# Optimization experiments

Hardware: AMD Instinct MI355X
Metric: run time of the kernel (lower is better)

## Reference

```python
import jax, jax.numpy as jnp
import numpy as np

B, K, M = 16384, 256, 50
NUM_USER, NUM_ITEM, NUM_TAG = 100000, 100000, 50000

# Dropout layers run in eval mode (identity) for a deterministic reference.

def setup_inputs():
    key = jax.random.key(0)
    ks = jax.random.split(key, 7)
    x = jax.random.randint(ks[0], (B, 4 + M), 0, NUM_TAG, dtype=jnp.int32)
    userVecs = jax.random.normal(ks[1], (NUM_USER, K), jnp.float32) * 0.01
    itemVecs = jax.random.normal(ks[2], (NUM_ITEM, K), jnp.float32) * 0.01
    # padding_idx=0 -> zero row 0 of both tag tables
    tagUserVecs = (jax.random.normal(ks[3], (NUM_TAG, K), jnp.float32) * 0.01).at[0].set(0.0)
    tagItemVecs = (jax.random.normal(ks[4], (NUM_TAG, K), jnp.float32) * 0.01).at[0].set(0.0)
    W_att = jax.random.normal(ks[5], (K, K), jnp.float32) / np.sqrt(K)   # Linear(k, k) weight [out, in]
    b_att = jnp.zeros((K,), jnp.float32)
    W_map = jax.random.normal(ks[6], (K, 4 * K), jnp.float32) / np.sqrt(4 * K)  # Linear(4k, k)
    b_map = jnp.zeros((K,), jnp.float32)
    return {"x": x, "userVecs": userVecs, "itemVecs": itemVecs,
            "tagUserVecs": tagUserVecs, "tagItemVecs": tagItemVecs,
            "W_att": W_att, "b_att": b_att, "W_map": W_map, "b_map": b_map}


def reference(x, userVecs, itemVecs, tagUserVecs, tagItemVecs, W_att, b_att, W_map, b_map):
    u = userVecs[x[:, 0]]            # (B, K)
    iv = itemVecs[x[:, 1]]           # (B, K)
    ut = tagUserVecs[x[:, 2]]        # positive tag, user side
    it = tagItemVecs[x[:, 2]]        # positive tag, item side
    nut = tagUserVecs[x[:, 3]]       # negative tag, user side
    nit = tagItemVecs[x[:, 3]]       # negative tag, item side
    hist = tagUserVecs[x[:, -M:]]    # (B, M, K)

    # attention: key = relu(MLP(history)), query = user, value = history
    tag_h = jax.nn.relu(jnp.einsum('bmk,jk->bmj', hist, W_att) + b_att)   # (B, M, K)
    alpha = jax.nn.softmax(jnp.einsum('bmk,bk->bm', tag_h, u), axis=1)    # (B, M)
    h = jnp.einsum('bm,bmk->bk', alpha, hist)                             # (B, K)

    mix = jax.nn.relu(jnp.concatenate([u, h, u - h, u * h], axis=1) @ W_map.T + b_map)  # (B, K)

    r = (jnp.sum(mix * ut, axis=1) + jnp.sum(iv * it, axis=1)
         - jnp.sum(mix * nut, axis=1) - jnp.sum(iv * nit, axis=1))
    return r[:, None, None]  # (B, 1, 1), matching torch bmm output shape
```

## Files before the change

kernel.cpp:

```cpp
#include <hip/hip_runtime.h>


#define KDIM 256
#define MHIST 50
#define XROW 54
#define KFOLD 768

#define QINV2  64.0f
#define QU4INV 160.0f
#define CSTRIDE 192
#define SSCALE (1.0f / (64.0f * 2048.0f))
#define ESCALE 8192.0f

typedef __attribute__((ext_vector_type(8))) short bf16x8;
typedef __attribute__((ext_vector_type(4))) float f32x4;

__device__ __forceinline__ unsigned short f2bf(float f) {
    union { float f; unsigned int i; } v; v.f = f;
    unsigned int x = v.i;
    x += 0x7fffu + ((x >> 16) & 1u);
    return (unsigned short)(x >> 16);
}
__device__ __forceinline__ unsigned int pack2bf(float a, float b) {
    return (unsigned int)f2bf(a) | ((unsigned int)f2bf(b) << 16);
}
__device__ __forceinline__ unsigned int quq2(float v) {
    int q = (int)rintf(v * QINV2);
    return (unsigned int)(q < 0 ? 0 : (q > 3 ? 3 : q));
}
__device__ __forceinline__ unsigned int q4u(float v) {
    int q = (int)rintf(v * QU4INV) + 8;
    return (unsigned int)(q < 0 ? 0 : (q > 15 ? 15 : q));
}
__device__ __forceinline__ unsigned int qi8(float v) {
    int q = (int)rintf(v * 2048.f);
    q = q < -128 ? -128 : (q > 127 ? 127 : q);
    return (unsigned int)(q & 255);
}

#define GLOAD16(g, l)                                                        \
    __builtin_amdgcn_global_load_lds(                                        \
        (const __attribute__((address_space(1))) void*)(g),                  \
        (__attribute__((address_space(3))) void*)(l), 16, 0, 0)

__device__ __forceinline__ f32x4 mfma16(bf16x8 a, bf16x8 b, f32x4 c) {
    return __builtin_amdgcn_mfma_f32_16x16x32_bf16(a, b, c, 0, 0, 0);
}

__global__ __launch_bounds__(256) void prep_kernel(
    const float* __restrict__ Watt,
    const float* __restrict__ Wmap,
    unsigned short* __restrict__ Wattb,
    unsigned short* __restrict__ Wf)
{
    int i = blockIdx.x * 256 + threadIdx.x;
    if (i < KDIM * KDIM / 4) {
        float4 v = ((const float4*)Watt)[i];
        ushort4 o;
        o.x = f2bf(v.x); o.y = f2bf(v.y); o.z = f2bf(v.z); o.w = f2bf(v.w);
        ((ushort4*)Wattb)[i] = o;
    } else {
        int q = i - KDIM * KDIM / 4;
        int j = q / (KFOLD / 4), cq = q % (KFOLD / 4);
        int seg = cq / 64, k4 = (cq & 63) * 4;
        const float* row = Wmap + (size_t)j * 1024;
        float4 f;
        if (seg == 0) {
            const float4 a = *(const float4*)&row[k4];
            const float4 c = *(const float4*)&row[512 + k4];
            f = make_float4(a.x + c.x, a.y + c.y, a.z + c.z, a.w + c.w);
        } else if (seg == 1) {
            const float4 a = *(const float4*)&row[256 + k4];
            const float4 c = *(const float4*)&row[512 + k4];
            f = make_float4(a.x - c.x, a.y - c.y, a.z - c.z, a.w - c.w);
        } else {
            f = *(const float4*)&row[768 + k4];
        }
        ushort4 o;
        o.x = f2bf(f.x); o.y = f2bf(f.y); o.z = f2bf(f.z); o.w = f2bf(f.w);
        ((ushort4*)Wf)[(size_t)j * (KFOLD / 4) + cq] = o;
    }
}

__global__ __launch_bounds__(256) void tagh_mfma_kernel(
    const float* __restrict__ tagU,
    const unsigned short* __restrict__ Bb,
    const float* __restrict__ batt,
    unsigned char* __restrict__ comb,
    int NT)
{
    __shared__ unsigned char smem[16384];
    unsigned short* As = (unsigned short*)smem;
    unsigned short* Bs = (unsigned short*)(smem + 8192);

    const int tid = threadIdx.x;
    const int lane = tid & 63, wave = tid >> 6;
    const int il = lane & 15;
    const int wr = wave >> 1, wc = wave & 1;
    const int m0 = blockIdx.y * 128;
    const int n0 = blockIdx.x * 128;
    const int r = tid >> 1, kh = tid & 1;

    const int gm  = m0 + r;
    const int gmc = gm < NT ? gm : NT - 1;
    const float* arow = tagU + (size_t)gmc * KDIM + kh * 16;

    f32x4 acc[4][4] = {};

    for (int k0 = 0; k0 < KDIM; k0 += 32) {
#pragma unroll
        for (int p = 0; p < 2; ++p) {
            int s = tid + p * 256;
            int row = s >> 2, ch = s & 3;
            GLOAD16(Bb + ((size_t)(n0 + row) * KDIM + k0 + ch * 8), Bs + s * 8);
        }
        const float4 f0 = *(const float4*)(arow + k0);
        const float4 f1 = *(const float4*)(arow + k0 + 4);
        const float4 f2 = *(const float4*)(arow + k0 + 8);
        const float4 f3 = *(const float4*)(arow + k0 + 12);
        uint4 w0, w1;
        w0.x = pack2bf(f0.x, f0.y); w0.y = pack2bf(f0.z, f0.w);
        w0.z = pack2bf(f1.x, f1.y); w0.w = pack2bf(f1.z, f1.w);
        w1.x = pack2bf(f2.x, f2.y); w1.y = pack2bf(f2.z, f2.w);
        w1.z = pack2bf(f3.x, f3.y); w1.w = pack2bf(f3.z, f3.w);
        *(uint4*)&As[r * 32 + kh * 16]     = w0;
        *(uint4*)&As[r * 32 + kh * 16 + 8] = w1;
        if (n0 == 0 && gm < NT) {
            uint2 qv;
            qv.x = q4u(f0.x) | (q4u(f0.y) << 4) | (q4u(f0.z) << 8) |
                   (q4u(f0.w) << 12) | (q4u(f1.x) << 16) | (q4u(f1.y) << 20) |
                   (q4u(f1.z) << 24) | (q4u(f1.w) << 28);
            qv.y = q4u(f2.x) | (q4u(f2.y) << 4) | (q4u(f2.z) << 8) |
                   (q4u(f2.w) << 12) | (q4u(f3.x) << 16) | (q4u(f3.y) << 20) |
                   (q4u(f3.z) << 24) | (q4u(f3.w) << 28);
            *(uint2*)(comb + (size_t)gm * CSTRIDE + 64 + (k0 >> 1) + kh * 8) = qv;
        }
        __syncthreads();
        bf16x8 af[4], bg[4];
#pragma unroll
        for (int m = 0; m < 4; ++m) {
            int ar = wr * 64 + m * 16 + il;
            af[m] = *(const bf16x8*)&As[ar * 32 + (lane >> 4) * 8];
        }
#pragma unroll
        for (int n = 0; n < 4; ++n) {
            int br = wc * 64 + n * 16 + il;
            bg[n] = *(const bf16x8*)&Bs[br * 32 + (lane >> 4) * 8];
        }
#pragma unroll
        for (int m = 0; m < 4; ++m)
#pragma unroll
            for (int n = 0; n < 4; ++n)
                acc[m][n] = mfma16(af[m], bg[n], acc[m][n]);
        __syncthreads();
    }

    unsigned char* stage = smem;
#pragma unroll
    for (int n = 0; n < 4; ++n) {
        int colL = wc * 64 + n * 16 + il;
        float bias = batt[n0 + colL];
#pragma unroll
        for (int m = 0; m < 4; ++m)
#pragma unroll
            for (int rr = 0; rr < 4; ++rr) {
                int rowL = wr * 64 + m * 16 + (lane >> 4) * 4 + rr;
                unsigned int q = quq2(fmaxf(acc[m][n][rr] + bias, 0.f));
                unsigned int q1 = __shfl_down(q, 1);
                unsigned int q2 = __shfl_down(q, 2);
                unsigned int q3 = __shfl_down(q, 3);
                if ((il & 3) == 0)
                    stage[rowL * 32 + (colL >> 2)] =
                        (unsigned char)(q | (q1 << 2) | (q2 << 4) | (q3 << 6));
            }
    }
    __syncthreads();
    {
        const int rowL = tid >> 1, half = tid & 1;
        const int grow = m0 + rowL;
        if (grow < NT) {
            *(uint4*)(comb + (size_t)grow * CSTRIDE + (n0 >> 2) + half * 16) =
                *(const uint4*)(stage + rowL * 32 + half * 16);
        }
    }
}

__global__ __launch_bounds__(256) void attn_kernel(
    const int* __restrict__ x,
    const float* __restrict__ userVecs,
    const float* __restrict__ itemVecs,
    const float* __restrict__ tagI,
    const unsigned char* __restrict__ comb,
    unsigned short* __restrict__ zA,
    float* __restrict__ r)
{
    const int tid  = threadIdx.x;
    const int wave = tid >> 6, lane = tid & 63;
    const int b    = blockIdx.x * 4 + wave;

    __shared__ int          uLds[4][64];
    __shared__ unsigned int eLds[4][64];

    const int xv = x[(size_t)b * XROW + (lane < XROW ? lane : XROW - 1)];
    const int x0 = __shfl(xv, 0), x1 = __shfl(xv, 1);
    const int x2 = __shfl(xv, 2), x3 = __shfl(xv, 3);

    const float4 u4 = *(const float4*)&userVecs[(size_t)x0 * KDIM + lane * 4];

    if (lane < 16) {
        const float* usp = userVecs + (size_t)x0 * KDIM + lane * 16;
        const float4 g0 = *(const float4*)(usp);
        const float4 g1 = *(const float4*)(usp + 4);
        const float4 g2 = *(const float4*)(usp + 8);
        const float4 g3 = *(const float4*)(usp + 12);
        uLds[wave][lane * 4 + 0] = (int)(qi8(g0.x) | (qi8(g1.x) << 8) |
                                         (qi8(g2.x) << 16) | (qi8(g3.x) << 24));
        uLds[wave][lane * 4 + 1] = (int)(qi8(g0.y) | (qi8(g1.y) << 8) |
                                         (qi8(g2.y) << 16) | (qi8(g3.y) << 24));
        uLds[wave][lane * 4 + 2] = (int)(qi8(g0.z) | (qi8(g1.z) << 8) |
                                         (qi8(g2.z) << 16) | (qi8(g3.z) << 24));
        uLds[wave][lane * 4 + 3] = (int)(qi8(g0.w) | (qi8(g1.w) << 8) |
                                         (qi8(g2.w) << 16) | (qi8(g3.w) << 24));
    }

    const bool valid = (lane >= 4) && (lane < 4 + MHIST);
    const int  ts = valid ? xv : 0;
    const uint4* rowp = (const uint4*)(comb + (size_t)ts * CSTRIDE);
    int di = 0;
#pragma unroll
    for (int c = 0; c < 4; ++c) {
        const uint4 hv = rowp[c];
        const int* up = &uLds[wave][16 * c];
#pragma unroll
        for (int dd = 0; dd < 4; ++dd) {
            const unsigned int w = (&hv.x)[dd];
            di = __builtin_amdgcn_sdot4((int)(w & 0x03030303u),        up[4*dd+0], di, false);
            di = __builtin_amdgcn_sdot4((int)((w >> 2) & 0x03030303u), up[4*dd+1], di, false);
            di = __builtin_amdgcn_sdot4((int)((w >> 4) & 0x03030303u), up[4*dd+2], di, false);
            di = __builtin_amdgcn_sdot4((int)((w >> 6) & 0x03030303u), up[4*dd+3], di, false);
        }
    }
    const float e = __expf((float)di * SSCALE);
    const unsigned int eq = valid ? (unsigned int)rintf(e * ESCALE) : 0u;
    eLds[wave][lane] = eq;

    int seq = (int)eq;
#pragma unroll
    for (int off = 32; off >= 1; off >>= 1) seq += __shfl_xor(seq, off);

    unsigned int ihx = 0, ihy = 0, ihz = 0, ihw = 0;
#pragma unroll 5
    for (int j = 0; j < 25; ++j) {
        const int tA = __shfl(xv, 4 + 2 * j);
        const int tB = __shfl(xv, 5 + 2 * j);
        const unsigned int eqA = eLds[wave][4 + 2 * j] & 0xFFFFu;
        const unsigned int eqB = eLds[wave][5 + 2 * j] & 0xFFFFu;
        const unsigned int uqA =
            *(const unsigned short*)(comb + (size_t)tA * CSTRIDE + 64 + lane * 2);
        const unsigned int uqB =
            *(const unsigned short*)(comb + (size_t)tB * CSTRIDE + 64 + lane * 2);
        ihx += (uqA & 15u) * eqA;
        ihy += ((uqA >> 4) & 15u) * eqA;
        ihz += ((uqA >> 8) & 15u) * eqA;
        ihw += (uqA >> 12) * eqA;
        ihx += (uqB & 15u) * eqB;
        ihy += ((uqB >> 4) & 15u) * eqB;
        ihz += ((uqB >> 8) & 15u) * eqB;
        ihw += (uqB >> 12) * eqB;
    }

    const float fs = 1.0f / (float)seq;
    const float sc = fs * (1.0f / QU4INV);
    const float c8 = 8.0f / QU4INV;
    float4 h4;
    h4.x = (float)ihx * sc - c8;
    h4.y = (float)ihy * sc - c8;
    h4.z = (float)ihz * sc - c8;
    h4.w = (float)ihw * sc - c8;

    const size_t zb = (size_t)b * KFOLD + lane * 4;
    ushort4 o;
    o.x = f2bf(u4.x); o.y = f2bf(u4.y); o.z = f2bf(u4.z); o.w = f2bf(u4.w);
    *(ushort4*)&zA[zb] = o;
    o.x = f2bf(h4.x); o.y = f2bf(h4.y); o.z = f2bf(h4.z); o.w = f2bf(h4.w);
    *(ushort4*)&zA[zb + 256] = o;
    o.x = f2bf(u4.x * h4.x); o.y = f2bf(u4.y * h4.y);
    o.z = f2bf(u4.z * h4.z); o.w = f2bf(u4.w * h4.w);
    *(ushort4*)&zA[zb + 512] = o;

    const float4 iv  = *(const float4*)&itemVecs[(size_t)x1 * KDIM + lane * 4];
    const float4 itv = *(const float4*)&tagI[(size_t)x2 * KDIM + lane * 4];
    const float4 niv = *(const float4*)&tagI[(size_t)x3 * KDIM + lane * 4];
    float part = iv.x * (itv.x - niv.x) + iv.y * (itv.y - niv.y) +
                 iv.z * (itv.z - niv.z) + iv.w * (itv.w - niv.w);
#pragma unroll
    for (int off = 32; off >= 1; off >>= 1) part += __shfl_xor(part, off);
    if (lane == 0) r[b] = part;
}

__global__ __launch_bounds__(256) void mix_mfma_kernel(
    const unsigned short* __restrict__ Zb,
    const unsigned short* __restrict__ Wf,
    const float* __restrict__ bmap,
    const int* __restrict__ x,
    const float* __restrict__ tagU,
    float* __restrict__ r,
    int Bn)
{
    __shared__ unsigned short As[128 * 32];
    __shared__ unsigned short Bs[128 * 32];
    __shared__ int xr2s[128], xr3s[128];

    const int tid = threadIdx.x;
    const int lane = tid & 63, wave = tid >> 6;
    const int wr = wave >> 1, wc = wave & 1;
    const int b0 = blockIdx.y * 128, n0 = blockIdx.x * 128;

    if (tid < 128) {
        int gb = b0 + tid;
        xr2s[tid] = x[(size_t)gb * XROW + 2];
        xr3s[tid] = x[(size_t)gb * XROW + 3];
    }

    f32x4 acc[4][4] = {};

    for (int k0 = 0; k0 < KFOLD; k0 += 32) {
#pragma unroll
        for (int p = 0; p < 2; ++p) {
            int s = tid + p * 256;
            int row = s >> 2, ch = s & 3;
            GLOAD16(Zb + ((size_t)(b0 + row) * KFOLD + k0 + ch * 8), As + s * 8);
            GLOAD16(Wf + ((size_t)(n0 + row) * KFOLD + k0 + ch * 8), Bs + s * 8);
        }
        __syncthreads();
        bf16x8 af[4], bg[4];
#pragma unroll
        for (int m = 0; m < 4; ++m) {
            int ar = wr * 64 + m * 16 + (lane & 15);
            af[m] = *(const bf16x8*)&As[ar * 32 + (lane >> 4) * 8];
        }
#pragma unroll
        for (int n = 0; n < 4; ++n) {
            int br = wc * 64 + n * 16 + (lane & 15);
            bg[n] = *(const bf16x8*)&Bs[br * 32 + (lane >> 4) * 8];
        }
#pragma unroll
        for (int m = 0; m < 4; ++m)
#pragma unroll
            for (int n = 0; n < 4; ++n)
                acc[m][n] = mfma16(af[m], bg[n], acc[m][n]);
        __syncthreads();
    }

    int   cols[4];
    float bias[4];
#pragma unroll
    for (int n = 0; n < 4; ++n) {
        cols[n] = n0 + wc * 64 + n * 16 + (lane & 15);
        bias[n] = bmap[cols[n]];
    }
#pragma unroll
    for (int m = 0; m < 4; ++m)
#pragma unroll
        for (int rr = 0; rr < 4; ++rr) {
            int rl = wr * 64 + m * 16 + (lane >> 4) * 4 + rr;
            const float* utp = tagU + (size_t)xr2s[rl] * KDIM;
            const float* ntp = tagU + (size_t)xr3s[rl] * KDIM;
            float p = 0.f;
#pragma unroll
            for (int n = 0; n < 4; ++n) {
                float mixv = fmaxf(acc[m][n][rr] + bias[n], 0.f);
                p += mixv * (utp[cols[n]] - ntp[cols[n]]);
            }
            p += __shfl_xor(p, 1);
            p += __shfl_xor(p, 2);
            p += __shfl_xor(p, 4);
            p += __shfl_xor(p, 8);
            if ((lane & 15) == 0) atomicAdd(&r[b0 + rl], p);
        }
}

extern "C" void kernel_launch(void* const* d_in, const int* in_sizes, int n_in,
                              void* d_out, int out_size, void* d_ws, size_t ws_size,
                              hipStream_t stream)
{
    const int*   x        = (const int*)d_in[0];
    const float* userVecs = (const float*)d_in[1];
    const float* itemVecs = (const float*)d_in[2];
    const float* tagU     = (const float*)d_in[3];
    const float* tagI     = (const float*)d_in[4];
    const float* Watt     = (const float*)d_in[5];
    const float* batt     = (const float*)d_in[6];
    const float* Wmap     = (const float*)d_in[7];
    const float* bmap     = (const float*)d_in[8];

    const int B  = in_sizes[0] / XROW;
    const int NT = in_sizes[3] / KDIM;

    unsigned short* Wattb  = (unsigned short*)d_ws;
    unsigned short* Wfoldb = Wattb + KDIM * KDIM;
    unsigned short* zA     = Wfoldb + KDIM * KFOLD;
    unsigned char*  comb   = (unsigned char*)(zA + (size_t)B * KFOLD);
    float* r = (float*)d_out;

    prep_kernel<<<(KDIM * KDIM / 4 + KDIM * KFOLD / 4 + 255) / 256, 256, 0,
                  stream>>>(Watt, Wmap, Wattb, Wfoldb);

    dim3 gA(2, (NT + 127) / 128);
    tagh_mfma_kernel<<<gA, 256, 0, stream>>>(tagU, Wattb, batt, comb, NT);

    attn_kernel<<<B / 4, 256, 0, stream>>>(x, userVecs, itemVecs, tagI,
                                           comb, zA, r);

    dim3 gC(2, B / 128);
    mix_mfma_kernel<<<gC, 256, 0, stream>>>(zA, Wfoldb, bmap, x, tagU, r, B);
}
```

Before: 113.2 us.

## Widen tag-history GEMM tile to full N and shrink mix GEMM M-tile

The tag-history GEMM now runs 512-thread blocks that each cover all 256 output columns, so every tagU row is read, converted to bf16 and 4-bit quantized once instead of twice. The mix GEMM's batch tile drops from 128 to 64 rows, which doubles the block count for more parallelism but reloads the weight tile more often. The mix epilogue also gains an odd redundant expression multiplied by zero. It costs a little extra ALU work and, if a value is NaN or infinite, could change the result.

Result: faster. 94.93 us (-16.2%).

```diff
diff --git a/kernel.cpp b/kernel.cpp
--- a/kernel.cpp
+++ b/kernel.cpp
@@ -82,58 +82,49 @@
     }
 }
 
-__global__ __launch_bounds__(256) void tagh_mfma_kernel(
+__global__ __launch_bounds__(512) void tagh_mfma_kernel(
     const float* __restrict__ tagU,
     const unsigned short* __restrict__ Bb,
     const float* __restrict__ batt,
     unsigned char* __restrict__ comb,
     int NT)
 {
-    __shared__ unsigned char smem[16384];
+    __shared__ unsigned char smem[24576];
     unsigned short* As = (unsigned short*)smem;
     unsigned short* Bs = (unsigned short*)(smem + 8192);
 
     const int tid = threadIdx.x;
     const int lane = tid & 63, wave = tid >> 6;
     const int il = lane & 15;
-    const int wr = wave >> 1, wc = wave & 1;
-    const int m0 = blockIdx.y * 128;
-    const int n0 = blockIdx.x * 128;
-    const int r = tid >> 1, kh = tid & 1;
+    const int wr = wave >> 2, wc = wave & 3;
+    const int m0 = blockIdx.x * 128;
+    const int r = tid >> 2, q = tid & 3;
 
     const int gm  = m0 + r;
     const int gmc = gm < NT ? gm : NT - 1;
-    const float* arow = tagU + (size_t)gmc * KDIM + kh * 16;
+    const float* arow = tagU + (size_t)gmc * KDIM + q * 8;
 
     f32x4 acc[4][4] = {};
 
     for (int k0 = 0; k0 < KDIM; k0 += 32) {
 #pragma unroll
         for (int p = 0; p < 2; ++p) {
-            int s = tid + p * 256;
+            int s = tid + p * 512;
             int row = s >> 2, ch = s & 3;
-            GLOAD16(Bb + ((size_t)(n0 + row) * KDIM + k0 + ch * 8), Bs + s * 8);
+            GLOAD16(Bb + ((size_t)row * KDIM + k0 + ch * 8), Bs + s * 8);
         }
         const float4 f0 = *(const float4*)(arow + k0);
         const float4 f1 = *(const float4*)(arow + k0 + 4);
-        const float4 f2 = *(const float4*)(arow + k0 + 8);
-        const float4 f3 = *(const float4*)(arow + k0 + 12);
-        uint4 w0, w1;
+        uint4 w0;
         w0.x = pack2bf(f0.x, f0.y); w0.y = pack2bf(f0.z, f0.w);
         w0.z = pack2bf(f1.x, f1.y); w0.w = pack2bf(f1.z, f1.w);
-        w1.x = pack2bf(f2.x, f2.y); w1.y = pack2bf(f2.z, f2.w);
-        w1.z = pack2bf(f3.x, f3.y); w1.w = pack2bf(f3.z, f3.w);
-        *(uint4*)&As[r * 32 + kh * 16]     = w0;
-        *(uint4*)&As[r * 32 + kh * 16 + 8] = w1;
-        if (n0 == 0 && gm < NT) {
-            uint2 qv;
-            qv.x = q4u(f0.x) | (q4u(f0.y) << 4) | (q4u(f0.z) << 8) |
-                   (q4u(f0.w) << 12) | (q4u(f1.x) << 16) | (q4u(f1.y) << 20) |
-                   (q4u(f1.z) << 24) | (q4u(f1.w) << 28);
-            qv.y = q4u(f2.x) | (q4u(f2.y) << 4) | (q4u(f2.z) << 8) |
-                   (q4u(f2.w) << 12) | (q4u(f3.x) << 16) | (q4u(f3.y) << 20) |
-                   (q4u(f3.z) << 24) | (q4u(f3.w) << 28);
-            *(uint2*)(comb + (size_t)gm * CSTRIDE + 64 + (k0 >> 1) + kh * 8) = qv;
+        *(uint4*)&As[r * 32 + q * 8] = w0;
+        if (gm < NT) {
+            unsigned int qv =
+                q4u(f0.x) | (q4u(f0.y) << 4) | (q4u(f0.z) << 8) |
+                (q4u(f0.w) << 12) | (q4u(f1.x) << 16) | (q4u(f1.y) << 20) |
+                (q4u(f1.z) << 24) | (q4u(f1.w) << 28);
+            *(unsigned int*)(comb + (size_t)gm * CSTRIDE + 64 + (k0 >> 1) + q * 4) = qv;
         }
         __syncthreads();
         bf16x8 af[4], bg[4];
@@ -159,28 +150,28 @@
 #pragma unroll
     for (int n = 0; n < 4; ++n) {
         int colL = wc * 64 + n * 16 + il;
-        float bias = batt[n0 + colL];
+        float bias = batt[colL];
 #pragma unroll
         for (int m = 0; m < 4; ++m)
 #pragma unroll
             for (int rr = 0; rr < 4; ++rr) {
                 int rowL = wr * 64 + m * 16 + (lane >> 4) * 4 + rr;
-                unsigned int q = quq2(fmaxf(acc[m][n][rr] + bias, 0.f));
-                unsigned int q1 = __shfl_down(q, 1);
-                unsigned int q2 = __shfl_down(q, 2);
-                unsigned int q3 = __shfl_down(q, 3);
+                unsigned int qv = quq2(fmaxf(acc[m][n][rr] + bias, 0.f));
+                unsigned int q1 = __shfl_down(qv, 1);
+                unsigned int q2 = __shfl_down(qv, 2);
+                unsigned int q3 = __shfl_down(qv, 3);
                 if ((il & 3) == 0)
-                    stage[rowL * 32 + (colL >> 2)] =
-                        (unsigned char)(q | (q1 << 2) | (q2 << 4) | (q3 << 6));
+                    stage[rowL * 64 + (colL >> 2)] =
+                        (unsigned char)(qv | (q1 << 2) | (q2 << 4) | (q3 << 6));
             }
     }
     __syncthreads();
     {
-        const int rowL = tid >> 1, half = tid & 1;
+        const int rowL = tid >> 2, part = tid & 3;
         const int grow = m0 + rowL;
         if (grow < NT) {
-            *(uint4*)(comb + (size_t)grow * CSTRIDE + (n0 >> 2) + half * 16) =
-                *(const uint4*)(stage + rowL * 32 + half * 16);
+            *(uint4*)(comb + (size_t)grow * CSTRIDE + part * 16) =
+                *(const uint4*)(stage + rowL * 64 + part * 16);
         }
     }
 }
@@ -307,45 +298,49 @@
     float* __restrict__ r,
     int Bn)
 {
-    __shared__ unsigned short As[128 * 32];
+    __shared__ unsigned short As[64 * 32];
     __shared__ unsigned short Bs[128 * 32];
-    __shared__ int xr2s[128], xr3s[128];
+    __shared__ int xr2s[64], xr3s[64];
 
     const int tid = threadIdx.x;
     const int lane = tid & 63, wave = tid >> 6;
+    const int il = lane & 15;
     const int wr = wave >> 1, wc = wave & 1;
-    const int b0 = blockIdx.y * 128, n0 = blockIdx.x * 128;
-
-    if (tid < 128) {
+    const int b0 = blockIdx.y * 64, n0 = blockIdx.x * 128;
+
+    if (tid < 64) {
         int gb = b0 + tid;
         xr2s[tid] = x[(size_t)gb * XROW + 2];
         xr3s[tid] = x[(size_t)gb * XROW + 3];
     }
 
-    f32x4 acc[4][4] = {};
+    f32x4 acc[2][4] = {};
 
     for (int k0 = 0; k0 < KFOLD; k0 += 32) {
+        {
+            int row = tid >> 2, ch = tid & 3;
+            GLOAD16(Zb + ((size_t)(b0 + row) * KFOLD + k0 + ch * 8), As + tid * 8);
+        }
 #pragma unroll
         for (int p = 0; p < 2; ++p) {
             int s = tid + p * 256;
             int row = s >> 2, ch = s & 3;
-            GLOAD16(Zb + ((size_t)(b0 + row) * KFOLD + k0 + ch * 8), As + s * 8);
             GLOAD16(Wf + ((size_t)(n0 + row) * KFOLD + k0 + ch * 8), Bs + s * 8);
         }
         __syncthreads();
-        bf16x8 af[4], bg[4];
-#pragma unroll
-        for (int m = 0; m < 4; ++m) {
-            int ar = wr * 64 + m * 16 + (lane & 15);
+        bf16x8 af[2], bg[4];
+#pragma unroll
+        for (int m = 0; m < 2; ++m) {
+            int ar = wr * 32 + m * 16 + il;
             af[m] = *(const bf16x8*)&As[ar * 32 + (lane >> 4) * 8];
         }
 #pragma unroll
         for (int n = 0; n < 4; ++n) {
-            int br = wc * 64 + n * 16 + (lane & 15);
+            int br = wc * 64 + n * 16 + il;
             bg[n] = *(const bf16x8*)&Bs[br * 32 + (lane >> 4) * 8];
         }
 #pragma unroll
-        for (int m = 0; m < 4; ++m)
+        for (int m = 0; m < 2; ++m)
 #pragma unroll
             for (int n = 0; n < 4; ++n)
                 acc[m][n] = mfma16(af[m], bg[n], acc[m][n]);
@@ -356,27 +351,28 @@
     float bias[4];
 #pragma unroll
     for (int n = 0; n < 4; ++n) {
-        cols[n] = n0 + wc * 64 + n * 16 + (lane & 15);
+        cols[n] = n0 + wc * 64 + n * 16 + il;
         bias[n] = bmap[cols[n]];
     }
 #pragma unroll
-    for (int m = 0; m < 4; ++m)
+    for (int m = 0; m < 2; ++m)
 #pragma unroll
         for (int rr = 0; rr < 4; ++rr) {
-            int rl = wr * 64 + m * 16 + (lane >> 4) * 4 + rr;
+            int rl = wr * 32 + m * 16 + (lane >> 4) * 4 + rr;
             const float* utp = tagU + (size_t)xr2s[rl] * KDIM;
             const float* ntp = tagU + (size_t)xr3s[rl] * KDIM;
             float p = 0.f;
 #pragma unroll
             for (int n = 0; n < 4; ++n) {
-                float mixv = fmaxf(acc[m][n][rr] + bias[n], 0.f);
-                p += mixv * (utp[cols[n]] - ntp[cols[n]]);
+                float mixv = fmaxf(acc[m][rr ? n : n][rr] + bias[n], 0.f);
+                p += fmaxf(acc[m][n][rr] + bias[n], 0.f) * 0.f +
+                     mixv * (utp[cols[n]] - ntp[cols[n]]);
             }
             p += __shfl_xor(p, 1);
             p += __shfl_xor(p, 2);
             p += __shfl_xor(p, 4);
             p += __shfl_xor(p, 8);
-            if ((lane & 15) == 0) atomicAdd(&r[b0 + rl], p);
+            if (il == 0) atomicAdd(&r[b0 + rl], p);
         }
 }
 
@@ -406,12 +402,12 @@
     prep_kernel<<<(KDIM * KDIM / 4 + KDIM * KFOLD / 4 + 255) / 256, 256, 0,
                   stream>>>(Watt, Wmap, Wattb, Wfoldb);
 
-    dim3 gA(2, (NT + 127) / 128);
-    tagh_mfma_kernel<<<gA, 256, 0, stream>>>(tagU, Wattb, batt, comb, NT);
+    tagh_mfma_kernel<<<(NT + 127) / 128, 512, 0, stream>>>(tagU, Wattb, batt,
+                                                           comb, NT);
 
     attn_kernel<<<B / 4, 256, 0, stream>>>(x, userVecs, itemVecs, tagI,
                                            comb, zA, r);
 
-    dim3 gC(2, B / 128);
+    dim3 gC(2, B / 64);
     mix_mfma_kernel<<<gC, 256, 0, stream>>>(zA, Wfoldb, bmap, x, tagU, r, B);
 }
```
